# Kernel tuning notes

Hardware: AMD Instinct MI355X
Metric: run time of the kernel (lower is better)

The kernel has to match this reference:

```python
import jax, jax.numpy as jnp
import numpy as np

B = 4; N_LIG = 150; N_PROT = 550; N = 700
H = 128; HEADS = 4; KPH = 32; HPH = 32
L = 6; K = 48; EDGE_CH = 128; CUTOFF = 10.0
PROT_F = 27; NUM_CLASSES = 13
LOG2 = 0.6931471805599453
FLAT = N * H  # 89600, matches fc1 in_features


def ssp(x):
    # ShiftedSoftplus
    return jax.nn.softplus(x) - LOG2


def lin(x, w, b):
    # torch Linear convention: w is [out, in]
    return jnp.einsum('...i,oi->...o', x, w) + b


def setup_inputs() -> dict:
    key = jax.random.key(0)
    ki = iter(jax.random.split(key, 40))

    def nrm(shape, fan_in):
        return jax.random.normal(next(ki), shape, jnp.float32) / np.sqrt(fan_in).astype(np.float32)

    lig_pos = jax.random.normal(next(ki), (B, N_LIG, 3), jnp.float32) * 3.0
    lig_t = jax.random.randint(next(ki), (B, N_LIG, 1), 0, NUM_CLASSES).astype(jnp.float32)
    state = jnp.concatenate([lig_pos, lig_t], axis=-1)  # [B, N_LIG, 4]
    protein_pos_v = jnp.concatenate([
        jax.random.normal(next(ki), (B, N_PROT, 3), jnp.float32) * 3.0,
        jax.random.normal(next(ki), (B, N_PROT, PROT_F), jnp.float32)], axis=-1)  # [B, N_PROT, 30]

    inp = dict(state=state, protein_pos_v=protein_pos_v)
    inp['w_prot'] = nrm((H, PROT_F), PROT_F); inp['b_prot'] = jnp.zeros((H,), jnp.float32)
    inp['w_lig'] = nrm((H, NUM_CLASSES), NUM_CLASSES); inp['b_lig'] = jnp.zeros((H,), jnp.float32)
    # per-layer stacked encoder params (grouped 1x1 conv == per-head linear, no bias)
    inp['wq'] = nrm((L, HEADS, KPH, HPH), HPH)
    inp['wk'] = nrm((L, HEADS, KPH, HPH), HPH)
    inp['wv'] = nrm((L, HEADS, HPH, HPH), HPH)
    inp['wkn1_w'] = nrm((L, KPH, EDGE_CH), EDGE_CH); inp['wkn1_b'] = jnp.zeros((L, KPH), jnp.float32)
    inp['wkn2_w'] = nrm((L, KPH, KPH), KPH); inp['wkn2_b'] = jnp.zeros((L, KPH), jnp.float32)
    inp['wkl_w'] = nrm((L, KPH, KPH), KPH); inp['wkl_b'] = jnp.zeros((L, KPH), jnp.float32)
    inp['wvn1_w'] = nrm((L, HPH, EDGE_CH), EDGE_CH); inp['wvn1_b'] = jnp.zeros((L, HPH), jnp.float32)
    inp['wvn2_w'] = nrm((L, HPH, HPH), HPH); inp['wvn2_b'] = jnp.zeros((L, HPH), jnp.float32)
    inp['wvl_w'] = nrm((L, HPH, HPH), HPH); inp['wvl_b'] = jnp.zeros((L, HPH), jnp.float32)
    inp['cen_w'] = nrm((L, H, H), H); inp['cen_b'] = jnp.zeros((L, H), jnp.float32)
    inp['out_w'] = nrm((L, H, H), H); inp['out_b'] = jnp.zeros((L, H), jnp.float32)
    inp['ln_g'] = jnp.ones((L, H), jnp.float32); inp['ln_b'] = jnp.zeros((L, H), jnp.float32)
    inp['fc1_w'] = nrm((128, FLAT), FLAT); inp['fc1_b'] = jnp.zeros((128,), jnp.float32)
    inp['fc2_w'] = nrm((64, 128), 128); inp['fc2_b'] = jnp.zeros((64,), jnp.float32)
    inp['fc3_w'] = nrm((1, 64), 64); inp['fc3_b'] = jnp.zeros((1,), jnp.float32)
    return inp


def reference(state, protein_pos_v, w_prot, b_prot, w_lig, b_lig, wq, wk, wv,
              wkn1_w, wkn1_b, wkn2_w, wkn2_b, wkl_w, wkl_b,
              wvn1_w, wvn1_b, wvn2_w, wvn2_b, wvl_w, wvl_b,
              cen_w, cen_b, out_w, out_b, ln_g, ln_b,
              fc1_w, fc1_b, fc2_w, fc2_b, fc3_w, fc3_b):
    lig_pos = state[..., :3]
    lig_t = jax.lax.stop_gradient(state[..., 3]).astype(jnp.int32)
    lig_oh = jax.nn.one_hot(lig_t, NUM_CLASSES, dtype=jnp.float32)
    prot_pos = protein_pos_v[..., :3]
    prot_v = protein_pos_v[..., 3:]
    # compose_context: stable sort by batch -> protein atoms then ligand atoms per complex
    h = jnp.concatenate([lin(prot_v, w_prot, b_prot), lin(lig_oh, w_lig, b_lig)], axis=1)  # [B,N,H]
    pos = jnp.concatenate([prot_pos, lig_pos], axis=1)  # [B,N,3]
    # kNN graph (k nearest neighbors, no self loops), batched per complex
    d2 = jnp.sum((pos[:, :, None, :] - pos[:, None, :, :]) ** 2, axis=-1)  # [B,N,N]
    d2 = d2 + jnp.eye(N, dtype=d2.dtype) * 1e9
    _, nbr = jax.lax.top_k(-d2, K)  # [B,N,K]
    dist = jnp.sqrt(jnp.take_along_axis(d2, nbr, axis=2))  # [B,N,K]
    # Gaussian smearing of edge lengths
    offset = jnp.linspace(0.0, CUTOFF, EDGE_CH)
    coeff = -0.5 / (offset[1] - offset[0]) ** 2
    edge_attr = jnp.exp(coeff * (dist[..., None] - offset) ** 2)  # [B,N,K,E]
    gat = jax.vmap(lambda a, i: a[i])  # per-batch neighbor gather
    for l in range(L):
        xh = h.reshape(B, N, HEADS, HPH)
        q = jnp.einsum('bnhd,hkd->bnhk', xh, wq[l])
        kx = jnp.einsum('bnhd,hkd->bnhk', xh, wk[l])
        vx = jnp.einsum('bnhd,hkd->bnhk', xh, wv[l])
        w_k = lin(ssp(lin(edge_attr, wkn1_w[l], wkn1_b[l])), wkn2_w[l], wkn2_b[l])  # [B,N,K,KPH]
        keys_j = lin(w_k[:, :, :, None, :] * gat(kx, nbr), wkl_w[l], wkl_b[l])  # [B,N,K,heads,KPH]
        qk = jnp.einsum('bnhk,bnmhk->bnmh', q, keys_j)  # per-edge attention logits
        alpha = jax.nn.softmax(qk, axis=2)  # scatter_softmax over each node's K edges
        w_v = lin(ssp(lin(edge_attr, wvn1_w[l], wvn1_b[l])), wvn2_w[l], wvn2_b[l])  # [B,N,K,HPH]
        msg = lin(w_v[:, :, :, None, :] * gat(vx, nbr), wvl_w[l], wvl_b[l])  # [B,N,K,heads,HPH]
        aggr = jnp.einsum('bnmh,bnmhd->bnhd', alpha, msg).reshape(B, N, H)
        x = lin(h, cen_w[l], cen_b[l]) + aggr
        mu = jnp.mean(x, axis=-1, keepdims=True)
        var = jnp.var(x, axis=-1, keepdims=True)
        x = (x - mu) / jnp.sqrt(var + 1e-5) * ln_g[l] + ln_b[l]
        h = h + lin(ssp(x), out_w[l], out_b[l])  # residual per interaction block
    # decoup_batch + pad_tensor: constant 700 nodes/complex -> plain reshape
    x = h.reshape(B, FLAT)
    x = jax.nn.relu(lin(x, fc1_w, fc1_b))
    x = jax.nn.relu(lin(x, fc2_w, fc2_b))
    return lin(x, fc3_w, fc3_b)  # [B,1]
```

## Files before the change

kernel.cpp:

```cpp
#include <hip/hip_runtime.h>
#include <hip/hip_fp16.h>
#include <math.h>

constexpr int cB   = 4;
constexpr int cNL  = 150;
constexpr int cNP  = 550;
constexpr int cN   = 700;
constexpr int cH   = 128;
constexpr int cHeads = 4;
constexpr int cL   = 6;
constexpr int cK   = 48;
constexpr int cPF  = 27;
constexpr int cNC  = 13;
constexpr int cFLAT = cN * cH;
constexpr int cEdges = cB * cN * cK;

constexpr int   TABN = 4096;
#define TAB_DMAX 11.0f
#define TAB_HT   (TAB_DMAX / (float)(TABN - 1))
#define TAB_INV  ((float)(TABN - 1) / TAB_DMAX)

#define RBF_STEP (10.0f / 127.0f)
#define RBF_COEFF (-0.5f / (RBF_STEP * RBF_STEP))
#define LOG2F_C 0.69314718055994530942f

__device__ __forceinline__ float sspf(float x) {
    float ax = fabsf(x);
    return fmaxf(x, 0.0f) + __logf(1.0f + __expf(-ax)) - LOG2F_C;
}

__device__ __forceinline__ int mbcnt64(unsigned long long m) {
    return __builtin_amdgcn_mbcnt_hi((unsigned)(m >> 32),
           __builtin_amdgcn_mbcnt_lo((unsigned)m, 0));
}

__global__ void __launch_bounds__(256) k_init(
    const float* __restrict__ wq, const float* __restrict__ wk, const float* __restrict__ wv,
    const float* __restrict__ wkn1_w, const float* __restrict__ wvn1_w,
    const float* __restrict__ wkn2_w, const float* __restrict__ wvn2_w,
    const float* __restrict__ wvl_w,
    const float* __restrict__ cen_w, const float* __restrict__ out_w,
    float* __restrict__ wqT, float* __restrict__ wkT, float* __restrict__ wvT,
    float* __restrict__ w1Tk, float* __restrict__ w1Tv,
    float* __restrict__ w2Tk, float* __restrict__ w2Tv,
    float* __restrict__ wvlT,
    float* __restrict__ cenT, float* __restrict__ outT,
    const float* __restrict__ state, const float* __restrict__ ppv,
    const float* __restrict__ w_prot, const float* __restrict__ b_prot,
    const float* __restrict__ w_lig, const float* __restrict__ b_lig,
    float* __restrict__ h, float* __restrict__ pos)
{
    if (blockIdx.x < 1320) {
        int idx = blockIdx.x * 256 + threadIdx.x;
        if (idx < 3 * 24576) {
            int seg = idx / 24576, i = idx % 24576;
            const float* src = seg == 0 ? wq : (seg == 1 ? wk : wv);
            float* dst = seg == 0 ? wqT : (seg == 1 ? wkT : wvT);
            int l = i / 4096, r = i % 4096;
            int hh = r / 1024, r2 = r % 1024;
            int d = r2 / 32, k = r2 % 32;
            dst[i] = src[(((size_t)l * 4 + hh) * 32 + k) * 32 + d];
            return;
        }
        idx -= 3 * 24576;
        if (idx < 2 * 24576) {
            int seg = idx / 24576, i = idx % 24576;
            const float* src = seg == 0 ? wkn1_w : wvn1_w;
            float* dst = seg == 0 ? w1Tk : w1Tv;
            int l = i / 4096, r = i % 4096;
            int c = r / 32, o = r % 32;
            dst[i] = src[((size_t)l * 32 + o) * 128 + c];
            return;
        }
        idx -= 2 * 24576;
        if (idx < 3 * 6144) {
            int seg = idx / 6144, i = idx % 6144;
            const float* src = seg == 0 ? wkn2_w : (seg == 1 ? wvn2_w : wvl_w);
            float* dst = seg == 0 ? w2Tk : (seg == 1 ? w2Tv : wvlT);
            int l = i / 1024, r = i % 1024;
            int c = r / 32, o = r % 32;
            dst[i] = src[((size_t)l * 32 + o) * 32 + c];
            return;
        }
        idx -= 3 * 6144;
        int seg = idx / 98304, i = idx % 98304;
        const float* src = seg == 0 ? cen_w : out_w;
        float* dst = seg == 0 ? cenT : outT;
        int l = i / 16384, r = i % 16384;
        int ii = r / 128, o = r % 128;
        dst[i] = src[((size_t)l * 128 + o) * 128 + ii];
        return;
    }
    int rel = blockIdx.x - 1320;
    int node = rel * 2 + (threadIdx.x >> 7);
    int b = node / cN, n = node % cN;
    int o = threadIdx.x & 127;
    int lane = threadIdx.x & 63;
    float out;
    if (n < cNP) {
        const float* src = ppv + ((size_t)b * cNP + n) * 30;
        float v = (lane < 30) ? src[lane] : 0.f;
        float s = b_prot[o];
        #pragma unroll
        for (int f = 0; f < cPF; f++) s += w_prot[o * cPF + f] * __shfl(v, 3 + f);
        out = s;
        if (o < 3) pos[((size_t)b * cN + n) * 3 + o] = v;
    } else {
        int nl = n - cNP;
        const float* src = state + ((size_t)b * cNL + nl) * 4;
        float v = (lane < 4) ? src[lane] : 0.f;
        int t = (int)__shfl(v, 3);
        out = w_lig[o * cNC + t] + b_lig[o];
        if (o < 3) pos[((size_t)b * cN + n) * 3 + o] = v;
    }
    h[((size_t)b * cN + n) * cH + o] = out;
}

__global__ void __launch_bounds__(256) k_knn(
    const float* __restrict__ pos, int* __restrict__ nbr, float* __restrict__ dist,
    const float* __restrict__ w1Tk, const float* __restrict__ wkn1_b,
    const float* __restrict__ w2Tk, const float* __restrict__ wkn2_b,
    const float* __restrict__ w1Tv, const float* __restrict__ wvn1_b,
    const float* __restrict__ w2Tv, const float* __restrict__ wvn2_b,
    float* __restrict__ tabP,
    const float* __restrict__ hbuf,
    const float* __restrict__ wqT, const float* __restrict__ wkT, const float* __restrict__ wvT,
    float* __restrict__ q0, __half* __restrict__ kx0, __half* __restrict__ vx0)
{
    int tid = threadIdx.x;
    if (blockIdx.x < cN) {
        int lane = tid & 63;
        int node = blockIdx.x * 4 + (tid >> 6);
        int b = node / cN, n = node % cN;
        const float* pb = pos + (size_t)b * cN * 3;
        float px = pb[n * 3 + 0], py = pb[n * 3 + 1], pz = pb[n * 3 + 2];
        float d2v[11];
        #pragma unroll
        for (int s = 0; s < 11; s++) {
            int j = lane + s * 64;
            float d2 = 1e30f;
            if (j < cN) {
                float dx = pb[j * 3 + 0] - px;
                float dy = pb[j * 3 + 1] - py;
                float dz = pb[j * 3 + 2] - pz;
                d2 = dx * dx + dy * dy + dz * dz;
                if (j == n) d2 = 1e9f;
            }
            d2v[s] = d2;
        }
        unsigned p = 0;
        for (int bit = 30; bit >= 0; --bit) {
            unsigned t = p | (1u << bit);
            int cnt = 0;
            #pragma unroll
            for (int s = 0; s < 11; s++)
                cnt += __popcll(__ballot(__float_as_uint(d2v[s]) < t));
            if (cnt <= 47) p = t;
        }
        int c_lt = 0;
        #pragma unroll
        for (int s = 0; s < 11; s++)
            c_lt += __popcll(__ballot(__float_as_uint(d2v[s]) < p));
        int base = 0, ebase = c_lt, need = 48 - c_lt;
        #pragma unroll
        for (int s = 0; s < 11; s++) {
            unsigned u = __float_as_uint(d2v[s]);
            unsigned long long blt = __ballot(u < p);
            unsigned long long beq = __ballot(u == p);
            int posn = -1;
            int bl = mbcnt64(blt);
            if (u < p) posn = base + bl;
            base += __popcll(blt);
            int r = mbcnt64(beq);
            int cs = __popcll(beq);
            int take = need < cs ? need : cs;
            if (u == p && r < take) posn = ebase + r;
            ebase += take; need -= take;
            if (posn >= 0) {
                nbr[(size_t)node * cK + posn] = s * 64 + lane;
                dist[(size_t)node * cK + posn] = sqrtf(d2v[s]);
            }
        }
        return;
    }
    if (blockIdx.x < cN + TABN / 4) {
        int rel = blockIdx.x - cN;
        int lane = tid & 63;
        int e = rel * 4 + (tid >> 6);
        int side = lane >> 5, o = lane & 31;
        float d = (float)e * TAB_HT;
        float z = d * (127.0f / 10.0f);
        int c0 = (int)floorf(z) - 7;
        c0 = c0 < 0 ? 0 : (c0 > 112 ? 112 : c0);
        int i = lane & 15;
        float tt = d - RBF_STEP * (float)(c0 + i);
        float eav = __expf(RBF_COEFF * tt * tt);
        const float* w1T = (side ? w1Tv : w1Tk);
        const float* b1  = (side ? wvn1_b : wkn1_b);
        const float* w2T = (side ? w2Tv : w2Tk);
        const float* b2  = (side ? wvn2_b : wkn2_b);
        int srcb = side * 32;
        for (int l = 0; l < cL; l++) {
            float s = b1[l * 32 + o];
            const float* w1p = w1T + (size_t)l * 4096;
            #pragma unroll
            for (int ii = 0; ii < 16; ii++)
                s += w1p[(c0 + ii) * 32 + o] * __shfl(eav, ii);
            float t1 = sspf(s);
            float s2 = b2[l * 32 + o];
            const float* w2p = w2T + (size_t)l * 1024;
            #pragma unroll
            for (int cc = 0; cc < 32; cc++)
                s2 += w2p[cc * 32 + o] * __shfl(t1, srcb + cc);
            tabP[((((size_t)l * TABN + e) * 2 + side) * 32 + o) * 2] = s2;
            if (e > 0)
                tabP[((((size_t)l * TABN + (e - 1)) * 2 + side) * 32 + o) * 2 + 1] = s2;
        }
        return;
    }
    int bn = (blockIdx.x - cN - TABN / 4) * 2 + (tid >> 7);
    int o = tid & 127;
    int hh = o >> 5, kq = o & 31;
    float hval = hbuf[(size_t)bn * cH + o];
    size_t wo = ((size_t)0 * 4 + hh) * 1024;
    const float* bq = wqT + wo;
    const float* bk = wkT + wo;
    const float* bv = wvT + wo;
    int srcb = (hh & 1) * 32;
    float sq = 0.f, sk = 0.f, sv = 0.f;
    #pragma unroll
    for (int d = 0; d < 32; d++) {
        float x = __shfl(hval, srcb + d);
        sq += bq[d * 32 + kq] * x;
        sk += bk[d * 32 + kq] * x;
        sv += bv[d * 32 + kq] * x;
    }
    q0[(size_t)bn * cH + o] = sq;
    kx0[(size_t)bn * cH + o] = __float2half(sk);
    vx0[(size_t)bn * cH + o] = __float2half(sv);
}

__global__ void __launch_bounds__(256) k_attn(
    int l,
    const float* __restrict__ h_in, const float* __restrict__ qr,
    const __half* __restrict__ kxr, const __half* __restrict__ vxr,
    const int* __restrict__ nbr, const float* __restrict__ dist,
    const float* __restrict__ tabP,
    const float* __restrict__ wkl_w,
    const float* __restrict__ wvlT, const float* __restrict__ wvl_b,
    const float* __restrict__ cenT, const float* __restrict__ cen_b,
    const float* __restrict__ outT, const float* __restrict__ out_b,
    const float* __restrict__ ln_g, const float* __restrict__ ln_b,
    float* __restrict__ h_out,
    float* __restrict__ qw, __half* __restrict__ kxw, __half* __restrict__ vxw,
    const float* __restrict__ wqT, const float* __restrict__ wkT, const float* __restrict__ wvT)
{
    int tid = threadIdx.x;
    int g = tid >> 7;
    int o = tid & 127;
    int lane = tid & 63;
    int bn = blockIdx.x * 2 + g;
    int b = bn / cN;
    int hh = o >> 5, c = o & 31;
    int srcb = (hh & 1) * 32;
    int hi = lane >> 5;

    __shared__ float sh_h[2][cH];
    __shared__ float sh_qk[2][cK * cHeads];
    __shared__ float sh_t[2][cH];
    __shared__ int   sh_nb[2][cK];
    __shared__ int   sh_idx[2][cK];
    __shared__ float sh_frac[2][cK];
    __shared__ float red[2][4];

    sh_h[g][o] = h_in[(size_t)bn * cH + o];
    float qv = qr[(size_t)bn * cH + o];
    if (o < cK) {
        sh_nb[g][o] = nbr[(size_t)bn * cK + o];
        float d = dist[(size_t)bn * cK + o];
        float z = d * TAB_INV;
        int idx = (int)z;
        if (idx > TABN - 2) idx = TABN - 2;
        sh_idx[g][o] = idx;
        sh_frac[g][o] = fminf(z - (float)idx, 1.0f);
    }
    __syncthreads();

    const float* wklp = wkl_w + l * 1024;
    float qt = 0.f;
    #pragma unroll 8
    for (int k = 0; k < 32; k++) qt += __shfl(qv, srcb + k) * wklp[k * 32 + c];

    const __half* kxb = kxr + (size_t)b * cN * cH;
    const __half* vxb = vxr + (size_t)b * cN * cH;
    const float2* tab2 = (const float2*)tabP + (size_t)l * TABN * 64;

    #pragma unroll 4
    for (int m = 0; m < cK; m += 2) {
        int j0 = sh_nb[g][m], j1 = sh_nb[g][m + 1];
        float k0 = __half2float(kxb[(size_t)j0 * cH + o]);
        float k1 = __half2float(kxb[(size_t)j1 * cH + o]);
        int mm = m + hi;
        float2 tp = tab2[((size_t)sh_idx[g][mm] * 2 + 0) * 32 + c];
        float wmine = tp.x + sh_frac[g][mm] * (tp.y - tp.x);
        float wother = __shfl_xor(wmine, 32);
        float w0 = hi ? wother : wmine;
        float w1 = hi ? wmine : wother;
        float pa = qt * w0 * k0;
        float pb = qt * w1 * k1;
        float x = (c & 1) ? pb : pa;
        float y = (c & 1) ? pa : pb;
        x += __shfl_xor(y, 1);
        x += __shfl_xor(x, 2);
        x += __shfl_xor(x, 4);
        x += __shfl_xor(x, 8);
        x += __shfl_xor(x, 16);
        if (c < 2) sh_qk[g][(m + c) * cHeads + hh] = x;
    }
    __syncthreads();

    {
        float v1 = sh_qk[g][c * cHeads + hh];
        float v2 = (c < cK - 32) ? sh_qk[g][(32 + c) * cHeads + hh] : -1e30f;
        float mx = fmaxf(v1, v2);
        #pragma unroll
        for (int off = 16; off; off >>= 1) mx = fmaxf(mx, __shfl_xor(mx, off));
        float e1 = __expf(v1 - mx);
        float e2 = (c < cK - 32) ? __expf(v2 - mx) : 0.f;
        float s = e1 + e2;
        #pragma unroll
        for (int off = 16; off; off >>= 1) s += __shfl_xor(s, off);
        float inv = 1.0f / s;
        sh_qk[g][c * cHeads + hh] = e1 * inv;
        if (c < cK - 32) sh_qk[g][(32 + c) * cHeads + hh] = e2 * inv;
    }
    __syncthreads();

    float t0 = 0.f, t1 = 0.f;
    #pragma unroll 4
    for (int m = 0; m < cK; m += 2) {
        int j0 = sh_nb[g][m], j1 = sh_nb[g][m + 1];
        float v0 = __half2float(vxb[(size_t)j0 * cH + o]);
        float v1 = __half2float(vxb[(size_t)j1 * cH + o]);
        int mm = m + hi;
        float2 sp = tab2[((size_t)sh_idx[g][mm] * 2 + 1) * 32 + c];
        float wmine = sp.x + sh_frac[g][mm] * (sp.y - sp.x);
        float wother = __shfl_xor(wmine, 32);
        float w0 = hi ? wother : wmine;
        float w1 = hi ? wmine : wother;
        t0 += sh_qk[g][m * cHeads + hh] * (w0 * v0);
        t1 += sh_qk[g][(m + 1) * cHeads + hh] * (w1 * v1);
    }
    sh_t[g][o] = t0 + t1;
    __syncthreads();

    const float* wvlTp = wvlT + l * 1024;
    float aggr = wvl_b[l * 32 + c];
    #pragma unroll 8
    for (int i = 0; i < 32; i++) aggr += wvlTp[i * 32 + c] * sh_t[g][hh * 32 + i];

    const float* cenTp = cenT + (size_t)l * cH * cH;
    float x0 = 0.f, x1 = 0.f;
    #pragma unroll 4
    for (int i = 0; i < cH; i += 2) {
        x0 += cenTp[i * cH + o] * sh_h[g][i];
        x1 += cenTp[(i + 1) * cH + o] * sh_h[g][i + 1];
    }
    float x = cen_b[l * cH + o] + aggr + x0 + x1;

    float s1 = x, s2 = x * x;
    #pragma unroll
    for (int off = 32; off; off >>= 1) {
        s1 += __shfl_xor(s1, off);
        s2 += __shfl_xor(s2, off);
    }
    int wid = (o >> 6);
    if ((o & 63) == 0) { red[g][wid * 2] = s1; red[g][wid * 2 + 1] = s2; }
    __syncthreads();
    float tot1 = red[g][0] + red[g][2], tot2 = red[g][1] + red[g][3];
    float mu = tot1 * (1.0f / 128.0f);
    float var = tot2 * (1.0f / 128.0f) - mu * mu;
    float xn = (x - mu) * rsqrtf(var + 1e-5f);
    xn = xn * ln_g[l * cH + o] + ln_b[l * cH + o];
    float sx = sspf(xn);
    sh_t[g][o] = sx;
    __syncthreads();

    const float* outTp = outT + (size_t)l * cH * cH;
    float o0 = 0.f, o1 = 0.f;
    #pragma unroll 4
    for (int i = 0; i < cH; i += 2) {
        o0 += outTp[i * cH + o] * sh_t[g][i];
        o1 += outTp[(i + 1) * cH + o] * sh_t[g][i + 1];
    }
    float hnew = sh_h[g][o] + out_b[l * cH + o] + o0 + o1;
    h_out[(size_t)bn * cH + o] = hnew;

    if (l < cL - 1) {
        size_t wo = ((size_t)(l + 1) * 4 + hh) * 1024;
        const float* bq = wqT + wo;
        const float* bk = wkT + wo;
        const float* bv = wvT + wo;
        float sq = 0.f, sk = 0.f, sv = 0.f;
        #pragma unroll
        for (int d = 0; d < 32; d++) {
            float xv = __shfl(hnew, srcb + d);
            sq += bq[d * 32 + c] * xv;
            sk += bk[d * 32 + c] * xv;
            sv += bv[d * 32 + c] * xv;
        }
        qw[(size_t)bn * cH + o] = sq;
        kxw[(size_t)bn * cH + o] = __float2half(sk);
        vxw[(size_t)bn * cH + o] = __float2half(sv);
    }
}

__global__ void __launch_bounds__(256) k_fc1p(const float* __restrict__ hbuf,
                                              const float* __restrict__ w,
                                              float* __restrict__ partial)
{
    int o = blockIdx.x >> 2, qp = blockIdx.x & 3;
    int tid = threadIdx.x;
    constexpr int CH = cFLAT / 4;
    const float4* wr = (const float4*)(w + (size_t)o * cFLAT + qp * CH);
    float a[4] = {0.f, 0.f, 0.f, 0.f};
    for (int i = tid; i < CH / 4; i += 256) {
        float4 wv = wr[i];
        #pragma unroll
        for (int bb = 0; bb < 4; bb++) {
            float4 hv = ((const float4*)(hbuf + (size_t)bb * cFLAT + qp * CH))[i];
            a[bb] += wv.x * hv.x + wv.y * hv.y + wv.z * hv.z + wv.w * hv.w;
        }
    }
    #pragma unroll
    for (int off = 32; off; off >>= 1) {
        #pragma unroll
        for (int bb = 0; bb < 4; bb++) a[bb] += __shfl_xor(a[bb], off);
    }
    __shared__ float red[4][4];
    if ((tid & 63) == 0) {
        #pragma unroll
        for (int bb = 0; bb < 4; bb++) red[tid >> 6][bb] = a[bb];
    }
    __syncthreads();
    if (tid < 4) {
        float s = red[0][tid] + red[1][tid] + red[2][tid] + red[3][tid];
        partial[((size_t)o * 4 + qp) * 4 + tid] = s;
    }
}

__global__ void __launch_bounds__(512) k_head2(const float* __restrict__ partial,
                                               const float* __restrict__ fc1_b,
                                               const float* __restrict__ fc2_w,
                                               const float* __restrict__ fc2_b,
                                               const float* __restrict__ fc3_w,
                                               const float* __restrict__ fc3_b,
                                               float* __restrict__ out)
{
    int tid = threadIdx.x;
    __shared__ float y1[4][128];
    __shared__ float y2[4][64];
    {
        int bb = tid >> 7, o = tid & 127;
        float s = fc1_b[o];
        #pragma unroll
        for (int qp = 0; qp < 4; qp++) s += partial[((size_t)o * 4 + qp) * 4 + bb];
        y1[bb][o] = fmaxf(s, 0.f);
    }
    __syncthreads();
    if (tid < 256) {
        int bb = tid >> 6, o = tid & 63;
        float s = fc2_b[o];
        #pragma unroll 8
        for (int i = 0; i < 128; i++) s += fc2_w[o * 128 + i] * y1[bb][i];
        y2[bb][o] = fmaxf(s, 0.f);
    }
    __syncthreads();
    if (tid < 4) {
        float s = fc3_b[0];
        #pragma unroll 8
        for (int i = 0; i < 64; i++) s += fc3_w[i] * y2[tid][i];
        out[tid] = s;
    }
}

extern "C" void kernel_launch(void* const* d_in, const int* in_sizes, int n_in,
                              void* d_out, int out_size, void* d_ws, size_t ws_size,
                              hipStream_t stream) {
    const float* state  = (const float*)d_in[0];
    const float* ppv    = (const float*)d_in[1];
    const float* w_prot = (const float*)d_in[2];
    const float* b_prot = (const float*)d_in[3];
    const float* w_lig  = (const float*)d_in[4];
    const float* b_lig  = (const float*)d_in[5];
    const float* wq     = (const float*)d_in[6];
    const float* wk     = (const float*)d_in[7];
    const float* wv     = (const float*)d_in[8];
    const float* wkn1_w = (const float*)d_in[9];
    const float* wkn1_b = (const float*)d_in[10];
    const float* wkn2_w = (const float*)d_in[11];
    const float* wkn2_b = (const float*)d_in[12];
    const float* wkl_w  = (const float*)d_in[13];
    const float* wvn1_w = (const float*)d_in[15];
    const float* wvn1_b = (const float*)d_in[16];
    const float* wvn2_w = (const float*)d_in[17];
    const float* wvn2_b = (const float*)d_in[18];
    const float* wvl_w  = (const float*)d_in[19];
    const float* wvl_b  = (const float*)d_in[20];
    const float* cen_w  = (const float*)d_in[21];
    const float* cen_b  = (const float*)d_in[22];
    const float* out_w  = (const float*)d_in[23];
    const float* out_b  = (const float*)d_in[24];
    const float* ln_g   = (const float*)d_in[25];
    const float* ln_b   = (const float*)d_in[26];
    const float* fc1_w  = (const float*)d_in[27];
    const float* fc1_b  = (const float*)d_in[28];
    const float* fc2_w  = (const float*)d_in[29];
    const float* fc2_b  = (const float*)d_in[30];
    const float* fc3_w  = (const float*)d_in[31];
    const float* fc3_b  = (const float*)d_in[32];

    float* ws = (float*)d_ws;
    size_t off = 0;
    float* pos   = ws + off; off += (size_t)cB * cN * 3;
    float* h_a   = ws + off; off += (size_t)cB * cN * cH;
    float* h_b   = ws + off; off += (size_t)cB * cN * cH;
    float* qA    = ws + off; off += (size_t)cB * cN * cH;
    float* qB    = ws + off; off += (size_t)cB * cN * cH;
    __half* kA   = (__half*)(ws + off); off += (size_t)cB * cN * cH / 2;
    __half* vA   = (__half*)(ws + off); off += (size_t)cB * cN * cH / 2;
    __half* kB   = (__half*)(ws + off); off += (size_t)cB * cN * cH / 2;
    __half* vB   = (__half*)(ws + off); off += (size_t)cB * cN * cH / 2;
    float* distb = ws + off; off += (size_t)cEdges;
    int*   nbrb  = (int*)(ws + off); off += (size_t)cEdges;
    float* tabb  = ws + off; off += (size_t)cL * TABN * 64 * 2;
    float* wqT   = ws + off; off += 24576;
    float* wkT   = ws + off; off += 24576;
    float* wvT   = ws + off; off += 24576;
    float* w1Tk  = ws + off; off += 24576;
    float* w1Tv  = ws + off; off += 24576;
    float* w2Tk  = ws + off; off += 6144;
    float* w2Tv  = ws + off; off += 6144;
    float* wvlT  = ws + off; off += 6144;
    float* cenT  = ws + off; off += 98304;
    float* outT  = ws + off; off += 98304;
    float* partial = ws + off; off += 2048;

    k_init<<<2720, 256, 0, stream>>>(wq, wk, wv, wkn1_w, wvn1_w, wkn2_w, wvn2_w,
                                     wvl_w, cen_w, out_w,
                                     wqT, wkT, wvT, w1Tk, w1Tv, w2Tk, w2Tv, wvlT, cenT, outT,
                                     state, ppv, w_prot, b_prot, w_lig, b_lig, h_a, pos);
    k_knn<<<cN + TABN / 4 + cB * cN / 2, 256, 0, stream>>>(
        pos, nbrb, distb,
        w1Tk, wkn1_b, w2Tk, wkn2_b, w1Tv, wvn1_b, w2Tv, wvn2_b, tabb,
        h_a, wqT, wkT, wvT, qA, kA, vA);

    float* hc = h_a;
    float* hn = h_b;
    for (int l = 0; l < cL; l++) {
        float* qr = (l & 1) ? qB : qA;
        __half* kr = (l & 1) ? kB : kA;
        __half* vr = (l & 1) ? vB : vA;
        float* qw2 = (l & 1) ? qA : qB;
        __half* kw2 = (l & 1) ? kA : kB;
        __half* vw2 = (l & 1) ? vA : vB;
        k_attn<<<cB * cN / 2, 256, 0, stream>>>(l, hc, qr, kr, vr, nbrb, distb, tabb,
            wkl_w, wvlT, wvl_b, cenT, cen_b, outT, out_b, ln_g, ln_b,
            hn, qw2, kw2, vw2, wqT, wkT, wvT);
        float* tmp = hc; hc = hn; hn = tmp;
    }

    k_fc1p<<<512, 256, 0, stream>>>(hc, fc1_w, partial);
    k_head2<<<1, 512, 0, stream>>>(partial, fc1_b, fc2_w, fc2_b, fc3_w, fc3_b, (float*)d_out);
}
```

Measured before the change: 310.9 us.

## Process one node per wavefront in k_attn with paired-channel packed layouts

Restructures the attention/interaction kernel so each 64-lane wavefront handles a whole node (two channels per lane), with q/k/v stored in an interleaved pair layout and cen/out/wq/wk/wv weights pre-packed into float2 pair layouts at init. This removes the block-wide __syncthreads and shared-memory staging of h, neighbors and table indices, replacing them with wave shuffles and an LDS waitcnt. The aim is to cut synchronization and halve gather instructions via half2/float2 loads, at the cost of more registers per lane and four nodes per block.

```diff
diff --git a/kernel.cpp b/kernel.cpp
--- a/kernel.cpp
+++ b/kernel.cpp
@@ -41,16 +41,17 @@
     const float* __restrict__ wvl_w,
     const float* __restrict__ cen_w, const float* __restrict__ out_w,
     float* __restrict__ wqT, float* __restrict__ wkT, float* __restrict__ wvT,
+    float* __restrict__ wqP2, float* __restrict__ wkP2, float* __restrict__ wvP2,
     float* __restrict__ w1Tk, float* __restrict__ w1Tv,
     float* __restrict__ w2Tk, float* __restrict__ w2Tv,
     float* __restrict__ wvlT,
-    float* __restrict__ cenT, float* __restrict__ outT,
+    float* __restrict__ cenP2, float* __restrict__ outP2,
     const float* __restrict__ state, const float* __restrict__ ppv,
     const float* __restrict__ w_prot, const float* __restrict__ b_prot,
     const float* __restrict__ w_lig, const float* __restrict__ b_lig,
     float* __restrict__ h, float* __restrict__ pos)
 {
-    if (blockIdx.x < 1320) {
+    if (blockIdx.x < 1608) {
         int idx = blockIdx.x * 256 + threadIdx.x;
         if (idx < 3 * 24576) {
             int seg = idx / 24576, i = idx % 24576;
@@ -63,6 +64,17 @@
             return;
         }
         idx -= 3 * 24576;
+        if (idx < 3 * 24576) {
+            int seg = idx / 24576, i = idx % 24576;
+            const float* src = seg == 0 ? wq : (seg == 1 ? wk : wv);
+            float* dst = seg == 0 ? wqP2 : (seg == 1 ? wkP2 : wvP2);
+            int pair = i >> 1, z = i & 1;
+            int lane = pair & 63, d = (pair >> 6) & 31, l = pair >> 11;
+            int hh = (lane >> 5) + 2 * z, cc = lane & 31;
+            dst[i] = src[(((size_t)l * 4 + hh) * 32 + cc) * 32 + d];
+            return;
+        }
+        idx -= 3 * 24576;
         if (idx < 2 * 24576) {
             int seg = idx / 24576, i = idx % 24576;
             const float* src = seg == 0 ? wkn1_w : wvn1_w;
@@ -73,25 +85,35 @@
             return;
         }
         idx -= 2 * 24576;
-        if (idx < 3 * 6144) {
+        if (idx < 2 * 6144) {
             int seg = idx / 6144, i = idx % 6144;
-            const float* src = seg == 0 ? wkn2_w : (seg == 1 ? wvn2_w : wvl_w);
-            float* dst = seg == 0 ? w2Tk : (seg == 1 ? w2Tv : wvlT);
+            const float* src = seg == 0 ? wkn2_w : wvn2_w;
+            float* dst = seg == 0 ? w2Tk : w2Tv;
             int l = i / 1024, r = i % 1024;
             int c = r / 32, o = r % 32;
             dst[i] = src[((size_t)l * 32 + o) * 32 + c];
             return;
         }
-        idx -= 3 * 6144;
-        int seg = idx / 98304, i = idx % 98304;
-        const float* src = seg == 0 ? cen_w : out_w;
-        float* dst = seg == 0 ? cenT : outT;
-        int l = i / 16384, r = i % 16384;
-        int ii = r / 128, o = r % 128;
-        dst[i] = src[((size_t)l * 128 + o) * 128 + ii];
+        idx -= 2 * 6144;
+        if (idx < 6144) {
+            int i = idx;
+            int l = i / 1024, r = i % 1024;
+            int c = r / 32, o = r % 32;
+            wvlT[i] = wvl_w[((size_t)l * 32 + o) * 32 + c];
+            return;
+        }
+        idx -= 6144;
+        {
+            int seg = idx / 98304, f = idx % 98304;
+            const float* src = seg == 0 ? cen_w : out_w;
+            float* dst = seg == 0 ? cenP2 : outP2;
+            int pair = f >> 1, z = f & 1;
+            int j = pair & 63, ii = (pair >> 6) & 127, l = pair >> 13;
+            dst[f] = src[((size_t)l * 128 + j + z * 64) * 128 + ii];
+        }
         return;
     }
-    int rel = blockIdx.x - 1320;
+    int rel = blockIdx.x - 1608;
     int node = rel * 2 + (threadIdx.x >> 7);
     int b = node / cN, n = node % cN;
     int o = threadIdx.x & 127;
@@ -235,79 +257,79 @@
         sk += bk[d * 32 + kq] * x;
         sv += bv[d * 32 + kq] * x;
     }
-    q0[(size_t)bn * cH + o] = sq;
-    kx0[(size_t)bn * cH + o] = __float2half(sk);
-    vx0[(size_t)bn * cH + o] = __float2half(sv);
+    size_t pp = ((size_t)bn * 64 + (o & 63)) * 2 + (o >> 6);
+    q0[pp] = sq;
+    kx0[pp] = __float2half(sk);
+    vx0[pp] = __float2half(sv);
 }
 
 __global__ void __launch_bounds__(256) k_attn(
     int l,
-    const float* __restrict__ h_in, const float* __restrict__ qr,
-    const __half* __restrict__ kxr, const __half* __restrict__ vxr,
+    const float* __restrict__ h_in, const float* __restrict__ qrP,
+    const __half* __restrict__ kxrP, const __half* __restrict__ vxrP,
     const int* __restrict__ nbr, const float* __restrict__ dist,
     const float* __restrict__ tabP,
     const float* __restrict__ wkl_w,
     const float* __restrict__ wvlT, const float* __restrict__ wvl_b,
-    const float* __restrict__ cenT, const float* __restrict__ cen_b,
-    const float* __restrict__ outT, const float* __restrict__ out_b,
+    const float* __restrict__ cenP2, const float* __restrict__ cen_b,
+    const float* __restrict__ outP2, const float* __restrict__ out_b,
     const float* __restrict__ ln_g, const float* __restrict__ ln_b,
     float* __restrict__ h_out,
-    float* __restrict__ qw, __half* __restrict__ kxw, __half* __restrict__ vxw,
-    const float* __restrict__ wqT, const float* __restrict__ wkT, const float* __restrict__ wvT)
+    float* __restrict__ qwP, __half* __restrict__ kxwP, __half* __restrict__ vxwP,
+    const float* __restrict__ wqP2, const float* __restrict__ wkP2, const float* __restrict__ wvP2)
 {
     int tid = threadIdx.x;
-    int g = tid >> 7;
-    int o = tid & 127;
+    int wv = tid >> 6;
     int lane = tid & 63;
-    int bn = blockIdx.x * 2 + g;
+    int bn = blockIdx.x * 4 + wv;
     int b = bn / cN;
-    int hh = o >> 5, c = o & 31;
-    int srcb = (hh & 1) * 32;
-    int hi = lane >> 5;
-
-    __shared__ float sh_h[2][cH];
-    __shared__ float sh_qk[2][cK * cHeads];
-    __shared__ float sh_t[2][cH];
-    __shared__ int   sh_nb[2][cK];
-    __shared__ int   sh_idx[2][cK];
-    __shared__ float sh_frac[2][cK];
-    __shared__ float red[2][4];
-
-    sh_h[g][o] = h_in[(size_t)bn * cH + o];
-    float qv = qr[(size_t)bn * cH + o];
-    if (o < cK) {
-        sh_nb[g][o] = nbr[(size_t)bn * cK + o];
-        float d = dist[(size_t)bn * cK + o];
+    int c = lane & 31;
+    int hb = lane & 32;
+    int hlo = lane >> 5;
+
+    __shared__ float qkbuf[4][cHeads * cK];
+    float* qk = qkbuf[wv];
+
+    float h0 = h_in[(size_t)bn * cH + lane];
+    float h1 = h_in[(size_t)bn * cH + 64 + lane];
+    float2 q2 = ((const float2*)qrP)[(size_t)bn * 64 + lane];
+    int nbv = 0, idxv = 0; float fracv = 0.f;
+    if (lane < cK) {
+        nbv = nbr[(size_t)bn * cK + lane];
+        float d = dist[(size_t)bn * cK + lane];
         float z = d * TAB_INV;
         int idx = (int)z;
         if (idx > TABN - 2) idx = TABN - 2;
-        sh_idx[g][o] = idx;
-        sh_frac[g][o] = fminf(z - (float)idx, 1.0f);
-    }
-    __syncthreads();
+        idxv = idx;
+        fracv = fminf(z - (float)idx, 1.0f);
+    }
 
     const float* wklp = wkl_w + l * 1024;
-    float qt = 0.f;
+    float qt0 = 0.f, qt2 = 0.f;
     #pragma unroll 8
-    for (int k = 0; k < 32; k++) qt += __shfl(qv, srcb + k) * wklp[k * 32 + c];
-
-    const __half* kxb = kxr + (size_t)b * cN * cH;
-    const __half* vxb = vxr + (size_t)b * cN * cH;
+    for (int k = 0; k < 32; k++) {
+        float wk_ = wklp[k * 32 + c];
+        qt0 += wk_ * __shfl(q2.x, hb + k);
+        qt2 += wk_ * __shfl(q2.y, hb + k);
+    }
+
+    const __half2* kxb2 = (const __half2*)kxrP + (size_t)b * cN * 64;
+    const __half2* vxb2 = (const __half2*)vxrP + (size_t)b * cN * 64;
     const float2* tab2 = (const float2*)tabP + (size_t)l * TABN * 64;
 
     #pragma unroll 4
     for (int m = 0; m < cK; m += 2) {
-        int j0 = sh_nb[g][m], j1 = sh_nb[g][m + 1];
-        float k0 = __half2float(kxb[(size_t)j0 * cH + o]);
-        float k1 = __half2float(kxb[(size_t)j1 * cH + o]);
-        int mm = m + hi;
-        float2 tp = tab2[((size_t)sh_idx[g][mm] * 2 + 0) * 32 + c];
-        float wmine = tp.x + sh_frac[g][mm] * (tp.y - tp.x);
-        float wother = __shfl_xor(wmine, 32);
-        float w0 = hi ? wother : wmine;
-        float w1 = hi ? wmine : wother;
-        float pa = qt * w0 * k0;
-        float pb = qt * w1 * k1;
+        int j0 = __shfl(nbv, m), j1 = __shfl(nbv, m + 1);
+        int i0 = __shfl(idxv, m), i1 = __shfl(idxv, m + 1);
+        float f0 = __shfl(fracv, m), f1 = __shfl(fracv, m + 1);
+        __half2 k0p = kxb2[(size_t)j0 * 64 + lane];
+        __half2 k1p = kxb2[(size_t)j1 * 64 + lane];
+        float2 t0 = tab2[((size_t)i0 * 2 + 0) * 32 + c];
+        float2 t1 = tab2[((size_t)i1 * 2 + 0) * 32 + c];
+        float w0 = t0.x + f0 * (t0.y - t0.x);
+        float w1 = t1.x + f1 * (t1.y - t1.x);
+        float2 k0f = __half22float2(k0p), k1f = __half22float2(k1p);
+        float pa = qt0 * w0 * k0f.x, pb = qt0 * w1 * k1f.x;
         float x = (c & 1) ? pb : pa;
         float y = (c & 1) ? pa : pb;
         x += __shfl_xor(y, 1);
@@ -315,103 +337,136 @@
         x += __shfl_xor(x, 4);
         x += __shfl_xor(x, 8);
         x += __shfl_xor(x, 16);
-        if (c < 2) sh_qk[g][(m + c) * cHeads + hh] = x;
-    }
-    __syncthreads();
+        float pa2 = qt2 * w0 * k0f.y, pb2 = qt2 * w1 * k1f.y;
+        float x2 = (c & 1) ? pb2 : pa2;
+        float y2 = (c & 1) ? pa2 : pb2;
+        x2 += __shfl_xor(y2, 1);
+        x2 += __shfl_xor(x2, 2);
+        x2 += __shfl_xor(x2, 4);
+        x2 += __shfl_xor(x2, 8);
+        x2 += __shfl_xor(x2, 16);
+        if (c < 2) {
+            qk[hlo * cK + m + c] = x;
+            qk[(hlo + 2) * cK + m + c] = x2;
+        }
+    }
+    asm volatile("s_waitcnt lgkmcnt(0)" ::: "memory");
 
     {
-        float v1 = sh_qk[g][c * cHeads + hh];
-        float v2 = (c < cK - 32) ? sh_qk[g][(32 + c) * cHeads + hh] : -1e30f;
-        float mx = fmaxf(v1, v2);
-        #pragma unroll
-        for (int off = 16; off; off >>= 1) mx = fmaxf(mx, __shfl_xor(mx, off));
-        float e1 = __expf(v1 - mx);
-        float e2 = (c < cK - 32) ? __expf(v2 - mx) : 0.f;
-        float s = e1 + e2;
-        #pragma unroll
-        for (int off = 16; off; off >>= 1) s += __shfl_xor(s, off);
+        int sh = lane >> 4;
+        int mb = lane & 15;
+        float v0 = qk[sh * cK + mb];
+        float v1 = qk[sh * cK + mb + 16];
+        float v2 = qk[sh * cK + mb + 32];
+        float mx = fmaxf(v0, fmaxf(v1, v2));
+        #pragma unroll
+        for (int off = 8; off; off >>= 1) mx = fmaxf(mx, __shfl_xor(mx, off));
+        float e0 = __expf(v0 - mx), e1 = __expf(v1 - mx), e2 = __expf(v2 - mx);
+        float s = e0 + e1 + e2;
+        #pragma unroll
+        for (int off = 8; off; off >>= 1) s += __shfl_xor(s, off);
         float inv = 1.0f / s;
-        sh_qk[g][c * cHeads + hh] = e1 * inv;
-        if (c < cK - 32) sh_qk[g][(32 + c) * cHeads + hh] = e2 * inv;
-    }
-    __syncthreads();
-
-    float t0 = 0.f, t1 = 0.f;
+        qk[sh * cK + mb] = e0 * inv;
+        qk[sh * cK + mb + 16] = e1 * inv;
+        qk[sh * cK + mb + 32] = e2 * inv;
+    }
+    asm volatile("s_waitcnt lgkmcnt(0)" ::: "memory");
+
+    float tl = 0.f, th = 0.f, tl2 = 0.f, th2 = 0.f;
     #pragma unroll 4
     for (int m = 0; m < cK; m += 2) {
-        int j0 = sh_nb[g][m], j1 = sh_nb[g][m + 1];
-        float v0 = __half2float(vxb[(size_t)j0 * cH + o]);
-        float v1 = __half2float(vxb[(size_t)j1 * cH + o]);
-        int mm = m + hi;
-        float2 sp = tab2[((size_t)sh_idx[g][mm] * 2 + 1) * 32 + c];
-        float wmine = sp.x + sh_frac[g][mm] * (sp.y - sp.x);
-        float wother = __shfl_xor(wmine, 32);
-        float w0 = hi ? wother : wmine;
-        float w1 = hi ? wmine : wother;
-        t0 += sh_qk[g][m * cHeads + hh] * (w0 * v0);
-        t1 += sh_qk[g][(m + 1) * cHeads + hh] * (w1 * v1);
-    }
-    sh_t[g][o] = t0 + t1;
-    __syncthreads();
+        int j0 = __shfl(nbv, m), j1 = __shfl(nbv, m + 1);
+        int i0 = __shfl(idxv, m), i1 = __shfl(idxv, m + 1);
+        float f0 = __shfl(fracv, m), f1 = __shfl(fracv, m + 1);
+        __half2 v0p = vxb2[(size_t)j0 * 64 + lane];
+        __half2 v1p = vxb2[(size_t)j1 * 64 + lane];
+        float2 s0 = tab2[((size_t)i0 * 2 + 1) * 32 + c];
+        float2 s1 = tab2[((size_t)i1 * 2 + 1) * 32 + c];
+        float w0 = s0.x + f0 * (s0.y - s0.x);
+        float w1 = s1.x + f1 * (s1.y - s1.x);
+        float a0l = qk[hlo * cK + m], a1l = qk[hlo * cK + m + 1];
+        float a0h = qk[(hlo + 2) * cK + m], a1h = qk[(hlo + 2) * cK + m + 1];
+        float2 v0f = __half22float2(v0p), v1f = __half22float2(v1p);
+        tl  += a0l * (w0 * v0f.x);
+        tl2 += a1l * (w1 * v1f.x);
+        th  += a0h * (w0 * v0f.y);
+        th2 += a1h * (w1 * v1f.y);
+    }
+    tl += tl2; th += th2;
 
     const float* wvlTp = wvlT + l * 1024;
-    float aggr = wvl_b[l * 32 + c];
+    float ag_l = wvl_b[l * 32 + c];
+    float ag_h = ag_l;
     #pragma unroll 8
-    for (int i = 0; i < 32; i++) aggr += wvlTp[i * 32 + c] * sh_t[g][hh * 32 + i];
-
-    const float* cenTp = cenT + (size_t)l * cH * cH;
-    float x0 = 0.f, x1 = 0.f;
-    #pragma unroll 4
-    for (int i = 0; i < cH; i += 2) {
-        x0 += cenTp[i * cH + o] * sh_h[g][i];
-        x1 += cenTp[(i + 1) * cH + o] * sh_h[g][i + 1];
-    }
-    float x = cen_b[l * cH + o] + aggr + x0 + x1;
-
-    float s1 = x, s2 = x * x;
+    for (int i = 0; i < 32; i++) {
+        float w_ = wvlTp[i * 32 + c];
+        ag_l += w_ * __shfl(tl, hb + i);
+        ag_h += w_ * __shfl(th, hb + i);
+    }
+
+    const float2* cenp = (const float2*)cenP2 + (size_t)l * 8192;
+    float xl = cen_b[l * cH + lane] + ag_l;
+    float xh = cen_b[l * cH + 64 + lane] + ag_h;
+    float xl2 = 0.f, xh2 = 0.f;
+    #pragma unroll 8
+    for (int i = 0; i < 64; i++) {
+        float2 wp = cenp[(size_t)i * 64 + lane];
+        float hv = __shfl(h0, i);
+        xl += wp.x * hv; xh += wp.y * hv;
+        float2 wp2 = cenp[(size_t)(64 + i) * 64 + lane];
+        float hv2 = __shfl(h1, i);
+        xl2 += wp2.x * hv2; xh2 += wp2.y * hv2;
+    }
+    xl += xl2; xh += xh2;
+
+    float s1 = xl + xh, s2 = xl * xl + xh * xh;
     #pragma unroll
     for (int off = 32; off; off >>= 1) {
         s1 += __shfl_xor(s1, off);
         s2 += __shfl_xor(s2, off);
     }
-    int wid = (o >> 6);
-    if ((o & 63) == 0) { red[g][wid * 2] = s1; red[g][wid * 2 + 1] = s2; }
-    __syncthreads();
-    float tot1 = red[g][0] + red[g][2], tot2 = red[g][1] + red[g][3];
-    float mu = tot1 * (1.0f / 128.0f);
-    float var = tot2 * (1.0f / 128.0f) - mu * mu;
-    float xn = (x - mu) * rsqrtf(var + 1e-5f);
-    xn = xn * ln_g[l * cH + o] + ln_b[l * cH + o];
-    float sx = sspf(xn);
-    sh_t[g][o] = sx;
-    __syncthreads();
-
-    const float* outTp = outT + (size_t)l * cH * cH;
-    float o0 = 0.f, o1 = 0.f;
-    #pragma unroll 4
-    for (int i = 0; i < cH; i += 2) {
-        o0 += outTp[i * cH + o] * sh_t[g][i];
-        o1 += outTp[(i + 1) * cH + o] * sh_t[g][i + 1];
-    }
-    float hnew = sh_h[g][o] + out_b[l * cH + o] + o0 + o1;
-    h_out[(size_t)bn * cH + o] = hnew;
+    float mu = s1 * (1.0f / 128.0f);
+    float var = s2 * (1.0f / 128.0f) - mu * mu;
+    float rstd = rsqrtf(var + 1e-5f);
+    float sxl = sspf((xl - mu) * rstd * ln_g[l * cH + lane] + ln_b[l * cH + lane]);
+    float sxh = sspf((xh - mu) * rstd * ln_g[l * cH + 64 + lane] + ln_b[l * cH + 64 + lane]);
+
+    const float2* outp = (const float2*)outP2 + (size_t)l * 8192;
+    float ol = h0 + out_b[l * cH + lane];
+    float oh = h1 + out_b[l * cH + 64 + lane];
+    float ol2 = 0.f, oh2 = 0.f;
+    #pragma unroll 8
+    for (int i = 0; i < 64; i++) {
+        float2 wp = outp[(size_t)i * 64 + lane];
+        float sv_ = __shfl(sxl, i);
+        ol += wp.x * sv_; oh += wp.y * sv_;
+        float2 wp2 = outp[(size_t)(64 + i) * 64 + lane];
+        float sv2 = __shfl(sxh, i);
+        ol2 += wp2.x * sv2; oh2 += wp2.y * sv2;
+    }
+    ol += ol2; oh += oh2;
+    h_out[(size_t)bn * cH + lane] = ol;
+    h_out[(size_t)bn * cH + 64 + lane] = oh;
 
     if (l < cL - 1) {
-        size_t wo = ((size_t)(l + 1) * 4 + hh) * 1024;
-        const float* bq = wqT + wo;
-        const float* bk = wkT + wo;
-        const float* bv = wvT + wo;
-        float sq = 0.f, sk = 0.f, sv = 0.f;
-        #pragma unroll
+        const float2* wq2 = (const float2*)wqP2 + (size_t)(l + 1) * 2048;
+        const float2* wk2 = (const float2*)wkP2 + (size_t)(l + 1) * 2048;
+        const float2* wv2 = (const float2*)wvP2 + (size_t)(l + 1) * 2048;
+        float sql = 0.f, sqh = 0.f, skl = 0.f, skh = 0.f, svl = 0.f, svh = 0.f;
+        #pragma unroll 8
         for (int d = 0; d < 32; d++) {
-            float xv = __shfl(hnew, srcb + d);
-            sq += bq[d * 32 + c] * xv;
-            sk += bk[d * 32 + c] * xv;
-            sv += bv[d * 32 + c] * xv;
-        }
-        qw[(size_t)bn * cH + o] = sq;
-        kxw[(size_t)bn * cH + o] = __float2half(sk);
-        vxw[(size_t)bn * cH + o] = __float2half(sv);
+            float2 aq = wq2[(size_t)d * 64 + lane];
+            float2 ak = wk2[(size_t)d * 64 + lane];
+            float2 av = wv2[(size_t)d * 64 + lane];
+            float xlo = __shfl(ol, hb + d);
+            float xhi = __shfl(oh, hb + d);
+            sql += aq.x * xlo; sqh += aq.y * xhi;
+            skl += ak.x * xlo; skh += ak.y * xhi;
+            svl += av.x * xlo; svh += av.y * xhi;
+        }
+        ((float2*)qwP)[(size_t)bn * 64 + lane] = make_float2(sql, sqh);
+        ((__half2*)kxwP)[(size_t)bn * 64 + lane] = __floats2half2_rn(skl, skh);
+        ((__half2*)vxwP)[(size_t)bn * 64 + lane] = __floats2half2_rn(svl, svh);
     }
 }
 
@@ -537,19 +592,22 @@
     float* wqT   = ws + off; off += 24576;
     float* wkT   = ws + off; off += 24576;
     float* wvT   = ws + off; off += 24576;
+    float* wqP2  = ws + off; off += 24576;
+    float* wkP2  = ws + off; off += 24576;
+    float* wvP2  = ws + off; off += 24576;
     float* w1Tk  = ws + off; off += 24576;
     float* w1Tv  = ws + off; off += 24576;
     float* w2Tk  = ws + off; off += 6144;
     float* w2Tv  = ws + off; off += 6144;
     float* wvlT  = ws + off; off += 6144;
-    float* cenT  = ws + off; off += 98304;
-    float* outT  = ws + off; off += 98304;
+    float* cenP2 = ws + off; off += 98304;
+    float* outP2 = ws + off; off += 98304;
     float* partial = ws + off; off += 2048;
 
-    k_init<<<2720, 256, 0, stream>>>(wq, wk, wv, wkn1_w, wvn1_w, wkn2_w, wvn2_w,
-                                     wvl_w, cen_w, out_w,
-                                     wqT, wkT, wvT, w1Tk, w1Tv, w2Tk, w2Tv, wvlT, cenT, outT,
-                                     state, ppv, w_prot, b_prot, w_lig, b_lig, h_a, pos);
+    k_init<<<1608 + cB * cN / 2, 256, 0, stream>>>(
+        wq, wk, wv, wkn1_w, wvn1_w, wkn2_w, wvn2_w, wvl_w, cen_w, out_w,
+        wqT, wkT, wvT, wqP2, wkP2, wvP2, w1Tk, w1Tv, w2Tk, w2Tv, wvlT, cenP2, outP2,
+        state, ppv, w_prot, b_prot, w_lig, b_lig, h_a, pos);
     k_knn<<<cN + TABN / 4 + cB * cN / 2, 256, 0, stream>>>(
         pos, nbrb, distb,
         w1Tk, wkn1_b, w2Tk, wkn2_b, w1Tv, wvn1_b, w2Tv, wvn2_b, tabb,
@@ -564,9 +622,9 @@
         float* qw2 = (l & 1) ? qA : qB;
         __half* kw2 = (l & 1) ? kA : kB;
         __half* vw2 = (l & 1) ? vA : vB;
-        k_attn<<<cB * cN / 2, 256, 0, stream>>>(l, hc, qr, kr, vr, nbrb, distb, tabb,
-            wkl_w, wvlT, wvl_b, cenT, cen_b, outT, out_b, ln_g, ln_b,
-            hn, qw2, kw2, vw2, wqT, wkT, wvT);
+        k_attn<<<cB * cN / 4, 256, 0, stream>>>(l, hc, qr, kr, vr, nbrb, distb, tabb,
+            wkl_w, wvlT, wvl_b, cenP2, cen_b, outP2, out_b, ln_g, ln_b,
+            hn, qw2, kw2, vw2, wqP2, wkP2, wvP2);
         float* tmp = hc; hc = hn; hn = tmp;
     }
 
```

After: 382.6 us. 1.23x slower.

## Use one node per 128-thread block and replace block barriers with wave-local waits

Applied to the files above, without the earlier changes.

The attention kernel now runs one node per 128-thread block instead of two nodes per 256-thread block. Two __syncthreads are replaced by s_waitcnt lgkmcnt(0), which relies on each head's LDS data being produced and consumed within the same wave. A third barrier is removed by passing the aggregated values through lane shuffles instead of shared memory. The aim is to cut barrier stalls and LDS traffic. In exchange the grid doubles and correctness depends on the wave-local data layout staying as it is.

```diff
diff --git a/kernel.cpp b/kernel.cpp
--- a/kernel.cpp
+++ b/kernel.cpp
@@ -240,7 +240,7 @@
     vx0[(size_t)bn * cH + o] = __float2half(sv);
 }
 
-__global__ void __launch_bounds__(256) k_attn(
+__global__ void __launch_bounds__(128) k_attn(
     int l,
     const float* __restrict__ h_in, const float* __restrict__ qr,
     const __half* __restrict__ kxr, const __half* __restrict__ vxr,
@@ -255,34 +255,32 @@
     float* __restrict__ qw, __half* __restrict__ kxw, __half* __restrict__ vxw,
     const float* __restrict__ wqT, const float* __restrict__ wkT, const float* __restrict__ wvT)
 {
-    int tid = threadIdx.x;
-    int g = tid >> 7;
-    int o = tid & 127;
-    int lane = tid & 63;
-    int bn = blockIdx.x * 2 + g;
+    int o = threadIdx.x;
+    int lane = o & 63;
+    int bn = blockIdx.x;
     int b = bn / cN;
     int hh = o >> 5, c = o & 31;
     int srcb = (hh & 1) * 32;
     int hi = lane >> 5;
 
-    __shared__ float sh_h[2][cH];
-    __shared__ float sh_qk[2][cK * cHeads];
-    __shared__ float sh_t[2][cH];
-    __shared__ int   sh_nb[2][cK];
-    __shared__ int   sh_idx[2][cK];
-    __shared__ float sh_frac[2][cK];
-    __shared__ float red[2][4];
-
-    sh_h[g][o] = h_in[(size_t)bn * cH + o];
+    __shared__ float sh_h[cH];
+    __shared__ float sh_t[cH];
+    __shared__ float sh_qk[cK * cHeads];
+    __shared__ int   sh_nb[cK];
+    __shared__ int   sh_idx[cK];
+    __shared__ float sh_frac[cK];
+    __shared__ float red[2][2];
+
+    sh_h[o] = h_in[(size_t)bn * cH + o];
     float qv = qr[(size_t)bn * cH + o];
     if (o < cK) {
-        sh_nb[g][o] = nbr[(size_t)bn * cK + o];
+        sh_nb[o] = nbr[(size_t)bn * cK + o];
         float d = dist[(size_t)bn * cK + o];
         float z = d * TAB_INV;
         int idx = (int)z;
         if (idx > TABN - 2) idx = TABN - 2;
-        sh_idx[g][o] = idx;
-        sh_frac[g][o] = fminf(z - (float)idx, 1.0f);
+        sh_idx[o] = idx;
+        sh_frac[o] = fminf(z - (float)idx, 1.0f);
     }
     __syncthreads();
 
@@ -297,12 +295,12 @@
 
     #pragma unroll 4
     for (int m = 0; m < cK; m += 2) {
-        int j0 = sh_nb[g][m], j1 = sh_nb[g][m + 1];
+        int j0 = sh_nb[m], j1 = sh_nb[m + 1];
         float k0 = __half2float(kxb[(size_t)j0 * cH + o]);
         float k1 = __half2float(kxb[(size_t)j1 * cH + o]);
         int mm = m + hi;
-        float2 tp = tab2[((size_t)sh_idx[g][mm] * 2 + 0) * 32 + c];
-        float wmine = tp.x + sh_frac[g][mm] * (tp.y - tp.x);
+        float2 tp = tab2[((size_t)sh_idx[mm] * 2 + 0) * 32 + c];
+        float wmine = tp.x + sh_frac[mm] * (tp.y - tp.x);
         float wother = __shfl_xor(wmine, 32);
         float w0 = hi ? wother : wmine;
         float w1 = hi ? wmine : wother;
@@ -315,13 +313,13 @@
         x += __shfl_xor(x, 4);
         x += __shfl_xor(x, 8);
         x += __shfl_xor(x, 16);
-        if (c < 2) sh_qk[g][(m + c) * cHeads + hh] = x;
-    }
-    __syncthreads();
+        if (c < 2) sh_qk[(m + c) * cHeads + hh] = x;
+    }
+    asm volatile("s_waitcnt lgkmcnt(0)" ::: "memory");
 
     {
-        float v1 = sh_qk[g][c * cHeads + hh];
-        float v2 = (c < cK - 32) ? sh_qk[g][(32 + c) * cHeads + hh] : -1e30f;
+        float v1 = sh_qk[c * cHeads + hh];
+        float v2 = (c < cK - 32) ? sh_qk[(32 + c) * cHeads + hh] : -1e30f;
         float mx = fmaxf(v1, v2);
         #pragma unroll
         for (int off = 16; off; off >>= 1) mx = fmaxf(mx, __shfl_xor(mx, off));
@@ -331,40 +329,39 @@
         #pragma unroll
         for (int off = 16; off; off >>= 1) s += __shfl_xor(s, off);
         float inv = 1.0f / s;
-        sh_qk[g][c * cHeads + hh] = e1 * inv;
-        if (c < cK - 32) sh_qk[g][(32 + c) * cHeads + hh] = e2 * inv;
-    }
-    __syncthreads();
+        sh_qk[c * cHeads + hh] = e1 * inv;
+        if (c < cK - 32) sh_qk[(32 + c) * cHeads + hh] = e2 * inv;
+    }
+    asm volatile("s_waitcnt lgkmcnt(0)" ::: "memory");
 
     float t0 = 0.f, t1 = 0.f;
     #pragma unroll 4
     for (int m = 0; m < cK; m += 2) {
-        int j0 = sh_nb[g][m], j1 = sh_nb[g][m + 1];
+        int j0 = sh_nb[m], j1 = sh_nb[m + 1];
         float v0 = __half2float(vxb[(size_t)j0 * cH + o]);
         float v1 = __half2float(vxb[(size_t)j1 * cH + o]);
         int mm = m + hi;
-        float2 sp = tab2[((size_t)sh_idx[g][mm] * 2 + 1) * 32 + c];
-        float wmine = sp.x + sh_frac[g][mm] * (sp.y - sp.x);
+        float2 sp = tab2[((size_t)sh_idx[mm] * 2 + 1) * 32 + c];
+        float wmine = sp.x + sh_frac[mm] * (sp.y - sp.x);
         float wother = __shfl_xor(wmine, 32);
         float w0 = hi ? wother : wmine;
         float w1 = hi ? wmine : wother;
-        t0 += sh_qk[g][m * cHeads + hh] * (w0 * v0);
-        t1 += sh_qk[g][(m + 1) * cHeads + hh] * (w1 * v1);
-    }
-    sh_t[g][o] = t0 + t1;
-    __syncthreads();
+        t0 += sh_qk[m * cHeads + hh] * (w0 * v0);
+        t1 += sh_qk[(m + 1) * cHeads + hh] * (w1 * v1);
+    }
+    float tt = t0 + t1;
 
     const float* wvlTp = wvlT + l * 1024;
     float aggr = wvl_b[l * 32 + c];
     #pragma unroll 8
-    for (int i = 0; i < 32; i++) aggr += wvlTp[i * 32 + c] * sh_t[g][hh * 32 + i];
+    for (int i = 0; i < 32; i++) aggr += wvlTp[i * 32 + c] * __shfl(tt, srcb + i);
 
     const float* cenTp = cenT + (size_t)l * cH * cH;
     float x0 = 0.f, x1 = 0.f;
     #pragma unroll 4
     for (int i = 0; i < cH; i += 2) {
-        x0 += cenTp[i * cH + o] * sh_h[g][i];
-        x1 += cenTp[(i + 1) * cH + o] * sh_h[g][i + 1];
+        x0 += cenTp[i * cH + o] * sh_h[i];
+        x1 += cenTp[(i + 1) * cH + o] * sh_h[i + 1];
     }
     float x = cen_b[l * cH + o] + aggr + x0 + x1;
 
@@ -374,26 +371,26 @@
         s1 += __shfl_xor(s1, off);
         s2 += __shfl_xor(s2, off);
     }
-    int wid = (o >> 6);
-    if ((o & 63) == 0) { red[g][wid * 2] = s1; red[g][wid * 2 + 1] = s2; }
+    int wid = o >> 6;
+    if (lane == 0) { red[wid][0] = s1; red[wid][1] = s2; }
     __syncthreads();
-    float tot1 = red[g][0] + red[g][2], tot2 = red[g][1] + red[g][3];
+    float tot1 = red[0][0] + red[1][0], tot2 = red[0][1] + red[1][1];
     float mu = tot1 * (1.0f / 128.0f);
     float var = tot2 * (1.0f / 128.0f) - mu * mu;
     float xn = (x - mu) * rsqrtf(var + 1e-5f);
     xn = xn * ln_g[l * cH + o] + ln_b[l * cH + o];
     float sx = sspf(xn);
-    sh_t[g][o] = sx;
+    sh_t[o] = sx;
     __syncthreads();
 
     const float* outTp = outT + (size_t)l * cH * cH;
     float o0 = 0.f, o1 = 0.f;
     #pragma unroll 4
     for (int i = 0; i < cH; i += 2) {
-        o0 += outTp[i * cH + o] * sh_t[g][i];
-        o1 += outTp[(i + 1) * cH + o] * sh_t[g][i + 1];
-    }
-    float hnew = sh_h[g][o] + out_b[l * cH + o] + o0 + o1;
+        o0 += outTp[i * cH + o] * sh_t[i];
+        o1 += outTp[(i + 1) * cH + o] * sh_t[i + 1];
+    }
+    float hnew = sh_h[o] + out_b[l * cH + o] + o0 + o1;
     h_out[(size_t)bn * cH + o] = hnew;
 
     if (l < cL - 1) {
@@ -564,7 +561,7 @@
         float* qw2 = (l & 1) ? qA : qB;
         __half* kw2 = (l & 1) ? kA : kB;
         __half* vw2 = (l & 1) ? vA : vB;
-        k_attn<<<cB * cN / 2, 256, 0, stream>>>(l, hc, qr, kr, vr, nbrb, distb, tabb,
+        k_attn<<<cB * cN, 128, 0, stream>>>(l, hc, qr, kr, vr, nbrb, distb, tabb,
             wkl_w, wvlT, wvl_b, cenT, cen_b, outT, out_b, ln_g, ln_b,
             hn, qw2, kw2, vw2, wqT, wkT, wvT);
         float* tmp = hc; hc = hn; hn = tmp;
```

Result: faster. 303.6 us (median of 2 runs) (-2.3%).
